# Performance work log

Hardware: AMD Instinct MI355X
Metric: run time of the kernel (lower is better)

## Reference

```python
import jax, jax.numpy as jnp
import numpy as np

N_NODES = 100000
N_EDGES = 1600000
F_IN = 128
HID = 64
EPS = 1e-5


def setup_inputs() -> dict:
    key = jax.random.key(0)
    ks = jax.random.split(key, 16)
    x = jax.random.normal(ks[0], (N_NODES, F_IN), dtype=jnp.float32)
    edge_index = jax.random.randint(ks[1], (2, N_EDGES), 0, N_NODES, dtype=jnp.int64)
    inp = {"x": x, "edge_index": edge_index}
    # GCN layers: layer 0 maps F_IN->HID, layers 1,2 map HID->HID
    dims = [(F_IN, HID), (HID, HID), (HID, HID)]
    for i, (fi, fo) in enumerate(dims):
        inp[f"W{i}"] = jax.random.normal(ks[2 + i], (fi, fo), dtype=jnp.float32) / np.sqrt(fi)
        inp[f"b{i}"] = jnp.zeros((fo,), dtype=jnp.float32)
        inp[f"g{i}"] = jnp.ones((fo,), dtype=jnp.float32)
        inp[f"bt{i}"] = jnp.zeros((fo,), dtype=jnp.float32)
    inp["lw1"] = jax.random.normal(ks[8], (HID, HID // 2), dtype=jnp.float32) / np.sqrt(HID)
    inp["lb1"] = jnp.zeros((HID // 2,), dtype=jnp.float32)
    inp["lw2"] = jax.random.normal(ks[9], (HID // 2, 1), dtype=jnp.float32) / np.sqrt(HID // 2)
    inp["lb2"] = jnp.zeros((1,), dtype=jnp.float32)
    return inp


def _gcn_norm(edge_index, n_nodes):
    # add self loops, symmetric normalization D^{-1/2}(A+I)D^{-1/2}
    loops = jnp.arange(n_nodes, dtype=edge_index.dtype)
    src = jnp.concatenate([edge_index[0], loops])
    dst = jnp.concatenate([edge_index[1], loops])
    deg = jax.ops.segment_sum(jnp.ones_like(dst, dtype=jnp.float32), dst, num_segments=n_nodes)
    dinv = jax.lax.rsqrt(deg)  # deg >= 1 thanks to self loops
    norm = dinv[src] * dinv[dst]  # [E+N]
    return src, dst, norm


def reference(x, edge_index, W0, b0, g0, bt0, W1, b1, g1, bt1, W2, b2, g2, bt2, lw1, lb1, lw2, lb2):
    n = x.shape[0]
    src, dst, norm = _gcn_norm(edge_index, n)
    layers = [(W0, b0, g0, bt0), (W1, b1, g1, bt1), (W2, b2, g2, bt2)]
    h = x
    for W, b, g, bt in layers:
        hw = h @ W                                  # [N, H] dense GEMM
        msg = hw[src] * norm[:, None]               # gather + scale, [E+N, H]
        agg = jax.ops.segment_sum(msg, dst, num_segments=n) + b  # scatter-add
        # BatchNorm1d (training-mode batch stats, biased var)
        mu = agg.mean(axis=0)
        var = agg.var(axis=0)
        h = (agg - mu) * jax.lax.rsqrt(var + EPS) * g + bt
        h = jax.nn.relu(h)                          # dropout = identity (inference)
    h = jax.nn.relu(h @ lw1 + lb1)
    out = h @ lw2 + lb2                             # [N, 1]
    return out[:, 0]
```

## Files before the change

### kernel.cpp

```cpp
#include <hip/hip_runtime.h>
#include <hip/hip_fp16.h>

#define HIDW 64
#define EPSV 1e-5f
#define CAP 32
#define GRP 512
#define CHUNK 4096
#define PSLOTS 40
#define NBIN_MAX 256
#define NCHUNK_MAX 512
#define NSLOT 64
#define OVFR 32768

__global__ __launch_bounds__(256) void k_zero(int* __restrict__ deg, int* __restrict__ ovfcnt,
                                              float* __restrict__ stats, int n) {
    int i = blockIdx.x * 256 + threadIdx.x;
    if (i < n) deg[i] = 0;
    if (i < 2) ovfcnt[i] = 0;
    if (i < 3 * NSLOT * 128) stats[i] = 0.f;
}

__global__ __launch_bounds__(256) void k_part(const int* __restrict__ srcv, const int* __restrict__ dstv,
                                              int2* __restrict__ pairs, unsigned char* __restrict__ cnts,
                                              int2* __restrict__ ovfl, int* __restrict__ ovfcnt,
                                              int e, int nchunk, int nbin) {
    __shared__ int lcnt[NBIN_MAX];
    int tid = threadIdx.x;
    int chunk = blockIdx.x;
    for (int i = tid; i < nbin; i += 256) lcnt[i] = 0;
    __syncthreads();
    int base = chunk * CHUNK;
#pragma unroll
    for (int t = 0; t < CHUNK / 256; ++t) {
        int i = base + t * 256 + tid;
        if (i < e) {
            int s = srcv[i];
            int d = dstv[i];
            int k = d >> 9;
            int slot = atomicAdd(&lcnt[k], 1);
            if (slot < PSLOTS) {
                pairs[((size_t)k * nchunk + chunk) * PSLOTS + slot] = make_int2(s, d);
            } else {
                int o = atomicAdd(&ovfcnt[0], 1);
                if (o < OVFR) ovfl[o] = make_int2(s, d);
            }
        }
    }
    __syncthreads();
    for (int i = tid; i < nbin; i += 256)
        cnts[(size_t)i * nchunk + chunk] = (unsigned char)min(lcnt[i], PSLOTS);
}

__global__ __launch_bounds__(256) void k_own(const int2* __restrict__ pairs, const unsigned char* __restrict__ cnts,
                                             int* __restrict__ deg, unsigned char* __restrict__ bcnt,
                                             int* __restrict__ csr, int2* __restrict__ ovfl,
                                             int* __restrict__ ovfcnt, int n, int nchunk) {
    __shared__ int lcnt[GRP];
    __shared__ int bkt[GRP * CAP];
    __shared__ unsigned char scnt[NCHUNK_MAX];
    int g = blockIdx.x;
    int tid = threadIdx.x;
    int nbase = g << 9;
    int nloc = min(GRP, n - nbase);
    for (int i = tid; i < GRP; i += 256) lcnt[i] = 0;
    for (int i = tid; i < nchunk; i += 256) scnt[i] = cnts[(size_t)g * nchunk + i];
    __syncthreads();
    const int2* pb = pairs + (size_t)g * nchunk * PSLOTS;
    int tot = nchunk * PSLOTS;
    for (int i = tid; i < tot; i += 256) {
        int c = i / PSLOTS;
        int s = i - c * PSLOTS;
        if (s < (int)scnt[c]) {
            int2 p = pb[i];
            int loc = p.y - nbase;
            int pos = atomicAdd(&lcnt[loc], 1);
            if (pos < CAP) {
                bkt[loc * CAP + pos] = p.x;
            } else {
                int o = atomicAdd(&ovfcnt[1], 1);
                if (o < OVFR) ovfl[OVFR + o] = p;
            }
        }
    }
    __syncthreads();
    int* csrb = csr + (size_t)nbase * CAP;
    for (int i = tid; i < nloc * CAP; i += 256) csrb[i] = bkt[i];
    for (int i = tid; i < nloc; i += 256) {
        int c = lcnt[i];
        deg[nbase + i] = c;
        bcnt[nbase + i] = (unsigned char)min(c, CAP);
    }
}

__global__ __launch_bounds__(256) void k_ovfdeg(const int2* __restrict__ ovfl, const int* __restrict__ ovfcnt,
                                                int* __restrict__ deg) {
    int m0 = min(ovfcnt[0], OVFR);
    for (int i = threadIdx.x; i < m0; i += 256) atomicAdd(&deg[ovfl[i].y], 1);
}

__global__ __launch_bounds__(256) void k_ovf(const __half* __restrict__ hw, const int2* __restrict__ ovfl,
                                             const int* __restrict__ ovfcnt, const int* __restrict__ deg,
                                             float* __restrict__ agg) {
    int m0 = min(ovfcnt[0], OVFR);
    int m1 = min(ovfcnt[1], OVFR);
    int tot = m0 + m1;
    if (tot == 0) return;
    int lane = threadIdx.x & 63;
    int w = (blockIdx.x * 256 + threadIdx.x) >> 6;
    for (; w < tot; w += gridDim.x * 4) {
        int2 p = (w < m0) ? ovfl[w] : ovfl[OVFR + (w - m0)];
        float wt = rsqrtf(1.0f + (float)deg[p.y]);
        atomicAdd(&agg[(size_t)p.y * HIDW + lane], __half2float(hw[(size_t)p.x * HIDW + lane]) * wt);
    }
}

__global__ __launch_bounds__(256) void k_count(const int* __restrict__ dstv, int* __restrict__ deg, int e) {
    int i = blockIdx.x * 256 + threadIdx.x;
    if (i < e) atomicAdd(&deg[dstv[i]], 1);
}

__global__ __launch_bounds__(256) void k_scan1(const int* __restrict__ deg, int* __restrict__ off,
                                               int* __restrict__ bsum, int n) {
    __shared__ int s[256];
    int tid = threadIdx.x;
    int i = blockIdx.x * 256 + tid;
    int v = (i < n) ? deg[i] : 0;
    s[tid] = v;
    __syncthreads();
    for (int o = 1; o < 256; o <<= 1) {
        int t = (tid >= o) ? s[tid - o] : 0;
        __syncthreads();
        s[tid] += t;
        __syncthreads();
    }
    if (i < n) off[i] = s[tid] - v;
    if (tid == 255) bsum[blockIdx.x] = s[255];
}

__global__ __launch_bounds__(512) void k_scan2(int* __restrict__ bsum, int nb) {
    __shared__ int s[512];
    int tid = threadIdx.x;
    int v = (tid < nb) ? bsum[tid] : 0;
    s[tid] = v;
    __syncthreads();
    for (int o = 1; o < 512; o <<= 1) {
        int t = (tid >= o) ? s[tid - o] : 0;
        __syncthreads();
        s[tid] += t;
        __syncthreads();
    }
    if (tid < nb) bsum[tid] = s[tid] - v;
}

__global__ __launch_bounds__(256) void k_scan3(int* __restrict__ off, const int* __restrict__ bsum, int n) {
    int i = blockIdx.x * 256 + threadIdx.x;
    if (i < n) off[i] += bsum[blockIdx.x];
}

__global__ __launch_bounds__(256) void k_fill2(const int* __restrict__ srcv, const int* __restrict__ dstv,
                                               int* __restrict__ roff, int* __restrict__ csr, int e) {
    int i = blockIdx.x * 256 + threadIdx.x;
    if (i < e) {
        int d = dstv[i];
        int p = atomicAdd(&roff[d], 1);
        csr[p] = srcv[i];
    }
}

template <int K, bool BN>
__global__ __launch_bounds__(256) void k_gemm(const float* __restrict__ h, const float* __restrict__ W,
                                              __half* __restrict__ hw, int n,
                                              const float* __restrict__ st, const float* __restrict__ g,
                                              const float* __restrict__ bt, float invn,
                                              const int* __restrict__ deg) {
    constexpr int KP = K + 4;
    constexpr int KQ = K / 4;
    __shared__ float sH[64 * KP];
    __shared__ float sW[K * 64];
    __shared__ float sM[128];
    __shared__ float sSc[HIDW];
    __shared__ float sSh[HIDW];
    int tid = threadIdx.x;
    int node0 = blockIdx.x * 64;

    if (BN) {
        if (tid < 128) {
            float t = 0.f;
#pragma unroll 8
            for (int s = 0; s < NSLOT; ++s) t += st[s * 128 + tid];
            sM[tid] = t;
        }
        __syncthreads();
        if (tid < HIDW) {
            float mu = sM[tid] * invn;
            float var = sM[HIDW + tid] * invn - mu * mu;
            var = fmaxf(var, 0.f);
            float rstd = rsqrtf(var + EPSV);
            float sc = rstd * g[tid];
            sSc[tid] = sc;
            sSh[tid] = bt[tid] - mu * sc;
        }
        __syncthreads();
    }

    for (int i = tid; i < K * 16; i += 256)
        ((float4*)sW)[i] = ((const float4*)W)[i];
    for (int i = tid; i < 64 * KQ; i += 256) {
        int row = i / KQ, kq = i % KQ;
        int nn = node0 + row;
        if (nn >= n) nn = n - 1;
        float4 v = ((const float4*)h)[(size_t)nn * KQ + kq];
        if (BN) {
            int c = 4 * kq;
            v.x = fmaxf(fmaf(v.x, sSc[c + 0], sSh[c + 0]), 0.f);
            v.y = fmaxf(fmaf(v.y, sSc[c + 1], sSh[c + 1]), 0.f);
            v.z = fmaxf(fmaf(v.z, sSc[c + 2], sSh[c + 2]), 0.f);
            v.w = fmaxf(fmaf(v.w, sSc[c + 3], sSh[c + 3]), 0.f);
        }
        ((float4*)(sH + row * KP))[kq] = v;
    }
    __syncthreads();

    int tx = tid & 15;
    int ny = tid >> 4;
    const float* hbase = sH + (4 * ny) * KP;

    float acc[4][4];
#pragma unroll
    for (int j = 0; j < 4; ++j)
#pragma unroll
        for (int c = 0; c < 4; ++c) acc[j][c] = 0.f;

#pragma unroll 2
    for (int kq = 0; kq < KQ; ++kq) {
        float4 w0 = ((const float4*)(sW + (4 * kq + 0) * 64))[tx];
        float4 w1 = ((const float4*)(sW + (4 * kq + 1) * 64))[tx];
        float4 w2 = ((const float4*)(sW + (4 * kq + 2) * 64))[tx];
        float4 w3 = ((const float4*)(sW + (4 * kq + 3) * 64))[tx];
#pragma unroll
        for (int j = 0; j < 4; ++j) {
            float4 hv = ((const float4*)(hbase + j * KP))[kq];
            acc[j][0] = fmaf(hv.x, w0.x, acc[j][0]);
            acc[j][1] = fmaf(hv.x, w0.y, acc[j][1]);
            acc[j][2] = fmaf(hv.x, w0.z, acc[j][2]);
            acc[j][3] = fmaf(hv.x, w0.w, acc[j][3]);
            acc[j][0] = fmaf(hv.y, w1.x, acc[j][0]);
            acc[j][1] = fmaf(hv.y, w1.y, acc[j][1]);
            acc[j][2] = fmaf(hv.y, w1.z, acc[j][2]);
            acc[j][3] = fmaf(hv.y, w1.w, acc[j][3]);
            acc[j][0] = fmaf(hv.z, w2.x, acc[j][0]);
            acc[j][1] = fmaf(hv.z, w2.y, acc[j][1]);
            acc[j][2] = fmaf(hv.z, w2.z, acc[j][2]);
            acc[j][3] = fmaf(hv.z, w2.w, acc[j][3]);
            acc[j][0] = fmaf(hv.w, w3.x, acc[j][0]);
            acc[j][1] = fmaf(hv.w, w3.y, acc[j][1]);
            acc[j][2] = fmaf(hv.w, w3.z, acc[j][2]);
            acc[j][3] = fmaf(hv.w, w3.w, acc[j][3]);
        }
    }

#pragma unroll
    for (int j = 0; j < 4; ++j) {
        int node = node0 + 4 * ny + j;
        if (node < n) {
            float dv = rsqrtf(1.0f + (float)deg[node]);
            __half2 p01 = __floats2half2_rn(acc[j][0] * dv, acc[j][1] * dv);
            __half2 p23 = __floats2half2_rn(acc[j][2] * dv, acc[j][3] * dv);
            uint2 r;
            r.x = *(unsigned int*)&p01;
            r.y = *(unsigned int*)&p23;
            ((uint2*)hw)[(size_t)node * 16 + tx] = r;
        }
    }
}

template <bool BUCKET>
__global__ __launch_bounds__(256) void k_gather(const __half* __restrict__ hw, const int* __restrict__ csr,
                                                const int* __restrict__ roff, const int* __restrict__ deg,
                                                const unsigned char* __restrict__ bcnt,
                                                const float* __restrict__ bias,
                                                float* __restrict__ agg, float* __restrict__ st, int n) {
    __shared__ float sS[4 * 64];
    __shared__ float sQ[4 * 64];
    int tid = threadIdx.x;
    int lane = tid & 63;
    int w = tid >> 6;
    int eh = lane >> 5;
    int c2 = lane & 31;
    int v = blockIdx.x * 4 + w;
    bool valid = (v < n);
    int vv = valid ? v : 0;
    int dcnt = deg[vv];
    float dv = rsqrtf(1.0f + (float)dcnt);
    int cnt;
    const int* base;
    if (BUCKET) {
        cnt = bcnt[vv];
        base = csr + (size_t)vv * CAP;
    } else {
        cnt = dcnt;
        base = csr + (roff[vv] - dcnt);
    }
    const __half2* hw2 = (const __half2*)hw;
    float2 acc;
    {
        float2 f = __half22float2(hw2[(size_t)vv * 32 + c2]);
        acc = (eh == 0) ? f : make_float2(0.f, 0.f);
    }
    for (int j0 = 0; j0 < cnt; j0 += 64) {
        int m = min(cnt - j0, 64);
        int idx = (lane < m) ? base[j0 + lane] : 0;
        int nfull = m >> 1;
        int p = 0;
        for (; p + 4 <= nfull; p += 4) {
            int a0 = __shfl(idx, 2 * (p + 0) + eh);
            int a1 = __shfl(idx, 2 * (p + 1) + eh);
            int a2 = __shfl(idx, 2 * (p + 2) + eh);
            int a3 = __shfl(idx, 2 * (p + 3) + eh);
            float2 f0 = __half22float2(hw2[(size_t)a0 * 32 + c2]);
            float2 f1 = __half22float2(hw2[(size_t)a1 * 32 + c2]);
            float2 f2 = __half22float2(hw2[(size_t)a2 * 32 + c2]);
            float2 f3 = __half22float2(hw2[(size_t)a3 * 32 + c2]);
            acc.x += (f0.x + f1.x) + (f2.x + f3.x);
            acc.y += (f0.y + f1.y) + (f2.y + f3.y);
        }
        for (; p < nfull; ++p) {
            int a = __shfl(idx, 2 * p + eh);
            float2 f = __half22float2(hw2[(size_t)a * 32 + c2]);
            acc.x += f.x;
            acc.y += f.y;
        }
        if (m & 1) {
            int a = __shfl(idx, m - 1);
            float2 f = __half22float2(hw2[(size_t)a * 32 + c2]);
            if (eh == 0) {
                acc.x += f.x;
                acc.y += f.y;
            }
        }
    }
    acc.x += __shfl_xor(acc.x, 32);
    acc.y += __shfl_xor(acc.y, 32);
    float2 b2 = ((const float2*)bias)[c2];
    float2 fin;
    fin.x = fmaf(dv, acc.x, b2.x);
    fin.y = fmaf(dv, acc.y, b2.y);
    if (valid && eh == 0) ((float2*)agg)[(size_t)vv * 32 + c2] = fin;
    if (eh == 0) {
        float sx = valid ? fin.x : 0.f;
        float sy = valid ? fin.y : 0.f;
        sS[w * 64 + 2 * c2 + 0] = sx;
        sS[w * 64 + 2 * c2 + 1] = sy;
        sQ[w * 64 + 2 * c2 + 0] = sx * sx;
        sQ[w * 64 + 2 * c2 + 1] = sy * sy;
    }
    __syncthreads();
    if (tid < 64) {
        float S = sS[tid] + sS[64 + tid] + sS[128 + tid] + sS[192 + tid];
        float Q = sQ[tid] + sQ[64 + tid] + sQ[128 + tid] + sQ[192 + tid];
        float* slot = st + (size_t)(blockIdx.x & (NSLOT - 1)) * 128;
        atomicAdd(&slot[tid], S);
        atomicAdd(&slot[64 + tid], Q);
    }
}

__global__ __launch_bounds__(256) void k_head(const float* __restrict__ h, const float* __restrict__ lw1,
                                              const float* __restrict__ lb1, const float* __restrict__ lw2,
                                              const float* __restrict__ lb2, float* __restrict__ out, int n,
                                              const float* __restrict__ st, const float* __restrict__ g,
                                              const float* __restrict__ bt, float invn) {
    __shared__ float sW[64 * 32];
    __shared__ float sb1[32];
    __shared__ float sw2[32];
    __shared__ float sM[128];
    __shared__ float sSc[HIDW];
    __shared__ float sSh[HIDW];
    int tid = threadIdx.x;
    for (int i = tid; i < 64 * 32; i += 256) sW[i] = lw1[i];
    if (tid < 32) {
        sb1[tid] = lb1[tid];
        sw2[tid] = lw2[tid];
    }
    if (tid < 128) {
        float t = 0.f;
#pragma unroll 8
        for (int s = 0; s < NSLOT; ++s) t += st[s * 128 + tid];
        sM[tid] = t;
    }
    __syncthreads();
    if (tid < HIDW) {
        float mu = sM[tid] * invn;
        float var = sM[HIDW + tid] * invn - mu * mu;
        var = fmaxf(var, 0.f);
        float rstd = rsqrtf(var + EPSV);
        float sc = rstd * g[tid];
        sSc[tid] = sc;
        sSh[tid] = bt[tid] - mu * sc;
    }
    __syncthreads();
    int nd = blockIdx.x * 256 + tid;
    if (nd >= n) return;
    float acc[32];
#pragma unroll
    for (int j = 0; j < 32; ++j) acc[j] = sb1[j];
    const float4* hr = (const float4*)(h + (size_t)nd * HIDW);
#pragma unroll 4
    for (int kc = 0; kc < 16; ++kc) {
        float4 h4 = hr[kc];
        int c = 4 * kc;
        h4.x = fmaxf(fmaf(h4.x, sSc[c + 0], sSh[c + 0]), 0.f);
        h4.y = fmaxf(fmaf(h4.y, sSc[c + 1], sSh[c + 1]), 0.f);
        h4.z = fmaxf(fmaf(h4.z, sSc[c + 2], sSh[c + 2]), 0.f);
        h4.w = fmaxf(fmaf(h4.w, sSc[c + 3], sSh[c + 3]), 0.f);
        const float* w0 = &sW[(c + 0) * 32];
        const float* w1 = &sW[(c + 1) * 32];
        const float* w2 = &sW[(c + 2) * 32];
        const float* w3 = &sW[(c + 3) * 32];
#pragma unroll
        for (int j = 0; j < 32; ++j) {
            float t = fmaf(h4.x, w0[j], fmaf(h4.y, w1[j], fmaf(h4.z, w2[j], h4.w * w3[j])));
            acc[j] += t;
        }
    }
    float o = lb2[0];
#pragma unroll
    for (int j = 0; j < 32; ++j) o = fmaf(fmaxf(acc[j], 0.f), sw2[j], o);
    out[nd] = o;
}

extern "C" void kernel_launch(void* const* d_in, const int* in_sizes, int n_in,
                              void* d_out, int out_size, void* d_ws, size_t ws_size,
                              hipStream_t stream) {
    const float* x = (const float*)d_in[0];
    const int* ei = (const int*)d_in[1];
    const float* W[3] = {(const float*)d_in[2], (const float*)d_in[6], (const float*)d_in[10]};
    const float* B[3] = {(const float*)d_in[3], (const float*)d_in[7], (const float*)d_in[11]};
    const float* G[3] = {(const float*)d_in[4], (const float*)d_in[8], (const float*)d_in[12]};
    const float* BT[3] = {(const float*)d_in[5], (const float*)d_in[9], (const float*)d_in[13]};
    const float* lw1 = (const float*)d_in[14];
    const float* lb1 = (const float*)d_in[15];
    const float* lw2 = (const float*)d_in[16];
    const float* lb2 = (const float*)d_in[17];
    float* out = (float*)d_out;

    const int n = in_sizes[0] / 128;
    const int e = in_sizes[1] / 2;
    const int* srcv = ei;
    const int* dstv = ei + e;
    const float invn = 1.0f / (float)n;
    const int nchunk = (e + CHUNK - 1) / CHUNK;
    const int nbin = (n + GRP - 1) / GRP;

    char* ws = (char*)d_ws;
    size_t off = 0;
    auto alloc = [&](size_t bytes) -> char* {
        off = (off + 511) & ~(size_t)511;
        char* p = ws + off;
        off += bytes;
        return p;
    };
    float* stats = (float*)alloc((size_t)3 * NSLOT * 128 * 4);
    int* ovfcnt = (int*)alloc(512);
    int2* ovfl = (int2*)alloc((size_t)2 * OVFR * 8);
    unsigned char* cnts = (unsigned char*)alloc((size_t)nbin * nchunk);
    unsigned char* bcnt = (unsigned char*)alloc((size_t)n);
    int* deg = (int*)alloc((size_t)n * 4);
    float* bufA = (float*)alloc((size_t)n * HIDW * 4);
    __half* bufB = (__half*)alloc((size_t)n * HIDW * 2);
    size_t commonOff = off;

    size_t needA = ((commonOff + 511) & ~(size_t)511) + (size_t)n * CAP * 4;
    size_t pairsBytes = (size_t)nbin * nchunk * PSLOTS * 8;
    bool useA = (needA <= ws_size) && (pairsBytes <= (size_t)n * HIDW * 4) &&
                (nchunk <= NCHUNK_MAX) && (nbin <= NBIN_MAX);

    const int gN = (n + 255) / 256;
    const int gG = (n + 63) / 64;
    const int gV = (n + 3) / 4;

    int2* pairs = (int2*)bufA;
    int* csrB = nullptr;
    int* roff = nullptr;
    int* bsum = nullptr;
    int* csrC = nullptr;

    if (useA) {
        csrB = (int*)alloc((size_t)n * CAP * 4);
        k_zero<<<gN, 256, 0, stream>>>(deg, ovfcnt, stats, n);
        k_part<<<nchunk, 256, 0, stream>>>(srcv, dstv, pairs, cnts, ovfl, ovfcnt, e, nchunk, nbin);
        k_own<<<nbin, 256, 0, stream>>>(pairs, cnts, deg, bcnt, csrB, ovfl, ovfcnt, n, nchunk);
        k_ovfdeg<<<1, 256, 0, stream>>>(ovfl, ovfcnt, deg);
    } else {
        roff = (int*)alloc((size_t)(n + 1) * 4);
        bsum = (int*)alloc(512 * 4);
        csrC = (int*)alloc((size_t)e * 4);
        k_zero<<<gN, 256, 0, stream>>>(deg, ovfcnt, stats, n);
        k_count<<<(e + 255) / 256, 256, 0, stream>>>(dstv, deg, e);
        k_scan1<<<gN, 256, 0, stream>>>(deg, roff, bsum, n);
        k_scan2<<<1, 512, 0, stream>>>(bsum, gN);
        k_scan3<<<gN, 256, 0, stream>>>(roff, bsum, n);
        k_fill2<<<(e + 255) / 256, 256, 0, stream>>>(srcv, dstv, roff, csrC, e);
    }

    for (int L = 0; L < 3; ++L) {
        float* stL = stats + (size_t)L * NSLOT * 128;
        if (L == 0)
            k_gemm<128, false><<<gG, 256, 0, stream>>>(x, W[0], bufB, n, nullptr, nullptr, nullptr, invn, deg);
        else
            k_gemm<64, true><<<gG, 256, 0, stream>>>(bufA, W[L], bufB, n, stats + (size_t)(L - 1) * NSLOT * 128,
                                                     G[L - 1], BT[L - 1], invn, deg);
        if (useA) {
            k_gather<true><<<gV, 256, 0, stream>>>(bufB, csrB, nullptr, deg, bcnt, B[L], bufA, stL, n);
            k_ovf<<<16, 256, 0, stream>>>(bufB, ovfl, ovfcnt, deg, bufA);
        } else {
            k_gather<false><<<gV, 256, 0, stream>>>(bufB, csrC, roff, deg, nullptr, B[L], bufA, stL, n);
        }
    }

    k_head<<<gN, 256, 0, stream>>>(bufA, lw1, lb1, lw2, lb2, out, n, stats + (size_t)2 * NSLOT * 128,
                                   G[2], BT[2], invn);
}
```

Baseline: 404.4 us.

## Slice hidden features into four column planes and gather per slice via grid.y

```diff
diff --git a/kernel.cpp b/kernel.cpp
--- a/kernel.cpp
+++ b/kernel.cpp
@@ -11,6 +11,7 @@
 #define NCHUNK_MAX 512
 #define NSLOT 64
 #define OVFR 32768
+#define NSLICE 4
 
 __global__ __launch_bounds__(256) void k_zero(int* __restrict__ deg, int* __restrict__ ovfcnt,
                                               float* __restrict__ stats, int n) {
@@ -100,17 +101,19 @@
 
 __global__ __launch_bounds__(256) void k_ovf(const __half* __restrict__ hw, const int2* __restrict__ ovfl,
                                              const int* __restrict__ ovfcnt, const int* __restrict__ deg,
-                                             float* __restrict__ agg) {
+                                             float* __restrict__ agg, int n) {
     int m0 = min(ovfcnt[0], OVFR);
     int m1 = min(ovfcnt[1], OVFR);
     int tot = m0 + m1;
     if (tot == 0) return;
     int lane = threadIdx.x & 63;
     int w = (blockIdx.x * 256 + threadIdx.x) >> 6;
+    int s = lane >> 4, c = lane & 15;
     for (; w < tot; w += gridDim.x * 4) {
         int2 p = (w < m0) ? ovfl[w] : ovfl[OVFR + (w - m0)];
         float wt = rsqrtf(1.0f + (float)deg[p.y]);
-        atomicAdd(&agg[(size_t)p.y * HIDW + lane], __half2float(hw[(size_t)p.x * HIDW + lane]) * wt);
+        float v = __half2float(hw[((size_t)s * n + p.x) * 16 + c]);
+        atomicAdd(&agg[(size_t)p.y * HIDW + lane], v * wt);
     }
 }
 
@@ -259,6 +262,7 @@
         }
     }
 
+    int sl = tx >> 2, q = tx & 3;
 #pragma unroll
     for (int j = 0; j < 4; ++j) {
         int node = node0 + 4 * ny + j;
@@ -269,24 +273,25 @@
             uint2 r;
             r.x = *(unsigned int*)&p01;
             r.y = *(unsigned int*)&p23;
-            ((uint2*)hw)[(size_t)node * 16 + tx] = r;
+            ((uint2*)hw)[((size_t)sl * n + node) * 4 + q] = r;
         }
     }
 }
 
 template <bool BUCKET>
-__global__ __launch_bounds__(256) void k_gather(const __half* __restrict__ hw, const int* __restrict__ csr,
-                                                const int* __restrict__ roff, const int* __restrict__ deg,
-                                                const unsigned char* __restrict__ bcnt,
-                                                const float* __restrict__ bias,
-                                                float* __restrict__ agg, float* __restrict__ st, int n) {
-    __shared__ float sS[4 * 64];
-    __shared__ float sQ[4 * 64];
+__global__ __launch_bounds__(256) void k_gats(const __half* __restrict__ hw, const int* __restrict__ csr,
+                                              const int* __restrict__ roff, const int* __restrict__ deg,
+                                              const unsigned char* __restrict__ bcnt,
+                                              const float* __restrict__ bias,
+                                              float* __restrict__ agg, float* __restrict__ st, int n) {
+    __shared__ float sS[4 * 16];
+    __shared__ float sQ[4 * 16];
     int tid = threadIdx.x;
     int lane = tid & 63;
     int w = tid >> 6;
-    int eh = lane >> 5;
-    int c2 = lane & 31;
+    int g = lane >> 3;
+    int cl = lane & 7;
+    int s = blockIdx.y;
     int v = blockIdx.x * 4 + w;
     bool valid = (v < n);
     int vv = valid ? v : 0;
@@ -301,66 +306,62 @@
         cnt = dcnt;
         base = csr + (roff[vv] - dcnt);
     }
-    const __half2* hw2 = (const __half2*)hw;
+    const __half2* hws = (const __half2*)(hw + (size_t)s * n * 16);
     float2 acc;
     {
-        float2 f = __half22float2(hw2[(size_t)vv * 32 + c2]);
-        acc = (eh == 0) ? f : make_float2(0.f, 0.f);
+        float2 f = __half22float2(hws[(size_t)vv * 8 + cl]);
+        acc = (g == 0) ? f : make_float2(0.f, 0.f);
     }
     for (int j0 = 0; j0 < cnt; j0 += 64) {
         int m = min(cnt - j0, 64);
-        int idx = (lane < m) ? base[j0 + lane] : 0;
-        int nfull = m >> 1;
-        int p = 0;
-        for (; p + 4 <= nfull; p += 4) {
-            int a0 = __shfl(idx, 2 * (p + 0) + eh);
-            int a1 = __shfl(idx, 2 * (p + 1) + eh);
-            int a2 = __shfl(idx, 2 * (p + 2) + eh);
-            int a3 = __shfl(idx, 2 * (p + 3) + eh);
-            float2 f0 = __half22float2(hw2[(size_t)a0 * 32 + c2]);
-            float2 f1 = __half22float2(hw2[(size_t)a1 * 32 + c2]);
-            float2 f2 = __half22float2(hw2[(size_t)a2 * 32 + c2]);
-            float2 f3 = __half22float2(hw2[(size_t)a3 * 32 + c2]);
-            acc.x += (f0.x + f1.x) + (f2.x + f3.x);
-            acc.y += (f0.y + f1.y) + (f2.y + f3.y);
-        }
-        for (; p < nfull; ++p) {
-            int a = __shfl(idx, 2 * p + eh);
-            float2 f = __half22float2(hw2[(size_t)a * 32 + c2]);
-            acc.x += f.x;
-            acc.y += f.y;
-        }
-        if (m & 1) {
-            int a = __shfl(idx, m - 1);
-            float2 f = __half22float2(hw2[(size_t)a * 32 + c2]);
-            if (eh == 0) {
+        int idx = (lane < m) ? __builtin_nontemporal_load(base + j0 + lane) : 0;
+        int k = 0;
+        for (; k + 16 <= m; k += 16) {
+            int a0 = __shfl(idx, k + g);
+            int a1 = __shfl(idx, k + 8 + g);
+            float2 f0 = __half22float2(hws[(size_t)a0 * 8 + cl]);
+            float2 f1 = __half22float2(hws[(size_t)a1 * 8 + cl]);
+            acc.x += f0.x + f1.x;
+            acc.y += f0.y + f1.y;
+        }
+        for (; k < m; k += 8) {
+            int a = __shfl(idx, k + g);
+            float2 f = __half22float2(hws[(size_t)a * 8 + cl]);
+            if (k + g < m) {
                 acc.x += f.x;
                 acc.y += f.y;
             }
         }
     }
+    acc.x += __shfl_xor(acc.x, 8);
+    acc.y += __shfl_xor(acc.y, 8);
+    acc.x += __shfl_xor(acc.x, 16);
+    acc.y += __shfl_xor(acc.y, 16);
     acc.x += __shfl_xor(acc.x, 32);
     acc.y += __shfl_xor(acc.y, 32);
-    float2 b2 = ((const float2*)bias)[c2];
+    float2 b2 = ((const float2*)bias)[s * 8 + cl];
     float2 fin;
     fin.x = fmaf(dv, acc.x, b2.x);
     fin.y = fmaf(dv, acc.y, b2.y);
-    if (valid && eh == 0) ((float2*)agg)[(size_t)vv * 32 + c2] = fin;
-    if (eh == 0) {
+    if (g == 0) {
+        if (valid) {
+            unsigned long long uv = *(unsigned long long*)&fin;
+            __builtin_nontemporal_store(uv, (unsigned long long*)(agg + (size_t)vv * HIDW + s * 16 + 2 * cl));
+        }
         float sx = valid ? fin.x : 0.f;
         float sy = valid ? fin.y : 0.f;
-        sS[w * 64 + 2 * c2 + 0] = sx;
-        sS[w * 64 + 2 * c2 + 1] = sy;
-        sQ[w * 64 + 2 * c2 + 0] = sx * sx;
-        sQ[w * 64 + 2 * c2 + 1] = sy * sy;
-    }
-    __syncthreads();
-    if (tid < 64) {
-        float S = sS[tid] + sS[64 + tid] + sS[128 + tid] + sS[192 + tid];
-        float Q = sQ[tid] + sQ[64 + tid] + sQ[128 + tid] + sQ[192 + tid];
+        sS[w * 16 + 2 * cl + 0] = sx;
+        sS[w * 16 + 2 * cl + 1] = sy;
+        sQ[w * 16 + 2 * cl + 0] = sx * sx;
+        sQ[w * 16 + 2 * cl + 1] = sy * sy;
+    }
+    __syncthreads();
+    if (tid < 16) {
+        float S = sS[tid] + sS[16 + tid] + sS[32 + tid] + sS[48 + tid];
+        float Q = sQ[tid] + sQ[16 + tid] + sQ[32 + tid] + sQ[48 + tid];
         float* slot = st + (size_t)(blockIdx.x & (NSLOT - 1)) * 128;
-        atomicAdd(&slot[tid], S);
-        atomicAdd(&slot[64 + tid], Q);
+        atomicAdd(&slot[s * 16 + tid], S);
+        atomicAdd(&slot[64 + s * 16 + tid], Q);
     }
 }
 
@@ -502,6 +503,7 @@
         k_fill2<<<(e + 255) / 256, 256, 0, stream>>>(srcv, dstv, roff, csrC, e);
     }
 
+    dim3 gSl(gV, NSLICE, 1);
     for (int L = 0; L < 3; ++L) {
         float* stL = stats + (size_t)L * NSLOT * 128;
         if (L == 0)
@@ -510,10 +512,10 @@
             k_gemm<64, true><<<gG, 256, 0, stream>>>(bufA, W[L], bufB, n, stats + (size_t)(L - 1) * NSLOT * 128,
                                                      G[L - 1], BT[L - 1], invn, deg);
         if (useA) {
-            k_gather<true><<<gV, 256, 0, stream>>>(bufB, csrB, nullptr, deg, bcnt, B[L], bufA, stL, n);
-            k_ovf<<<16, 256, 0, stream>>>(bufB, ovfl, ovfcnt, deg, bufA);
+            k_gats<true><<<gSl, 256, 0, stream>>>(bufB, csrB, nullptr, deg, bcnt, B[L], bufA, stL, n);
+            k_ovf<<<16, 256, 0, stream>>>(bufB, ovfl, ovfcnt, deg, bufA, n);
         } else {
-            k_gather<false><<<gV, 256, 0, stream>>>(bufB, csrC, roff, deg, nullptr, B[L], bufA, stL, n);
+            k_gats<false><<<gSl, 256, 0, stream>>>(bufB, csrC, roff, deg, nullptr, B[L], bufA, stL, n);
         }
     }
 
```

Result: slower. 697.7 us (+72.5%).
